# Optimization experiments

Measured on AMD Instinct MI355X. Metric: run time of the kernel, lower is better.

## Reference

```python
import jax, jax.numpy as jnp
import numpy as np

KH = KW = 3
STRIDE = 1
PAD = 1
DIL = 1
G = 4  # deformable groups


def setup_inputs() -> dict:
    key = jax.random.key(0)
    k1, k2, k3 = jax.random.split(key, 3)
    B, C, H, W = 8, 256, 64, 64
    K = KH * KW
    inp = jax.random.normal(k1, (B, C, H, W), dtype=jnp.float32)
    offset = jax.random.normal(k2, (B, 2 * G * K, H, W), dtype=jnp.float32)
    mask = jax.random.uniform(k3, (B, G * K, H, W), dtype=jnp.float32)
    return {"input": inp, "offset": offset, "mask": mask}


def _deform_sample(x, offset, mask):
    # x: [B,C,H,W]; offset: [B,2*G*K,Ho,Wo]; mask: [B,G*K,Ho,Wo]
    B, C, H, W = x.shape
    K = KH * KW
    Ho = (H + 2 * PAD - DIL * (KH - 1) - 1) // STRIDE + 1
    Wo = (W + 2 * PAD - DIL * (KW - 1) - 1) // STRIDE + 1
    Cg = C // G

    off = offset.reshape(B, G, K, 2, Ho, Wo)  # (dy, dx) per group/tap
    m = mask.reshape(B, G, K, Ho, Wo)

    # base sampling grid per kernel tap
    ky = (jnp.arange(KH) * DIL).repeat(KW)          # [K]
    kx = jnp.tile(jnp.arange(KW) * DIL, KH)          # [K]
    base_y = jnp.arange(Ho) * STRIDE - PAD           # [Ho]
    base_x = jnp.arange(Wo) * STRIDE - PAD           # [Wo]

    # sampling positions [B,G,K,Ho,Wo]
    py = base_y[None, None, None, :, None] + ky[None, None, :, None, None] + off[:, :, :, 0]
    px = base_x[None, None, None, None, :] + kx[None, None, :, None, None] + off[:, :, :, 1]

    y0 = jnp.floor(py).astype(jnp.int32)
    x0 = jnp.floor(px).astype(jnp.int32)
    ly = py - y0.astype(py.dtype)
    lx = px - x0.astype(px.dtype)

    xg = x.reshape(B, G, Cg, H * W)

    def gather(yy, xx, w):
        valid = (yy >= 0) & (yy < H) & (xx >= 0) & (xx < W)
        idx = jnp.clip(yy, 0, H - 1) * W + jnp.clip(xx, 0, W - 1)  # [B,G,K,Ho,Wo]
        g = jnp.take_along_axis(xg, idx.reshape(B, G, 1, -1), axis=3)
        g = g.reshape(B, G, Cg, K, Ho, Wo)
        return g * (w * valid.astype(w.dtype))[:, :, None]

    acc = gather(y0, x0, (1 - ly) * (1 - lx))
    acc = acc + gather(y0, x0 + 1, (1 - ly) * lx)
    acc = acc + gather(y0 + 1, x0, ly * (1 - lx))
    acc = acc + gather(y0 + 1, x0 + 1, ly * lx)

    # mask-weighted accumulation over kernel taps
    out = (acc * m[:, :, None]).sum(axis=3)  # [B,G,Cg,Ho,Wo]
    return out.reshape(B, C, Ho, Wo)


def reference(input, offset, mask):
    return _deform_sample(input, offset, mask)
```

## Files before the change

### kernel.cpp

```cpp
#include <hip/hip_runtime.h>
#include <hip/hip_fp16.h>

#define B_  8
#define C_  256
#define H_  64
#define W_  64
#define G_  4
#define CG_ 64
#define K_  9
#define HW_ (H_ * W_)

__global__ __launch_bounds__(256) void to_nhwc_f16(const float* __restrict__ in,
                                                   __half* __restrict__ out) {
  __shared__ unsigned int tile[32][65];
  const int b  = blockIdx.z;
  const int p0 = blockIdx.x * 64;
  const int c0 = blockIdx.y * 64;
  const int tid = threadIdx.x;
  const float* src = in + (size_t)b * C_ * HW_;
  __half* dst = out + (size_t)b * HW_ * C_;

  const int px = tid & 63;
  const int cp0 = tid >> 6;
#pragma unroll
  for (int i = 0; i < 8; ++i) {
    const int cp = cp0 + i * 4;
    const int c = c0 + cp * 2;
    const float v0 = src[(size_t)c * HW_ + p0 + px];
    const float v1 = src[(size_t)(c + 1) * HW_ + p0 + px];
    const unsigned int lo = (unsigned int)__half_as_ushort(__float2half(v0));
    const unsigned int hi = (unsigned int)__half_as_ushort(__float2half(v1));
    tile[cp][px] = lo | (hi << 16);
  }
  __syncthreads();

  const int cpair = tid & 31;
  const int pr0   = tid >> 5;
#pragma unroll
  for (int i = 0; i < 8; ++i) {
    const int p = pr0 + i * 8;
    *(unsigned int*)(dst + (size_t)(p0 + p) * C_ + c0 + 2 * cpair) = tile[cpair][p];
  }
}

__global__ __launch_bounds__(256) void deform_f16(const __half* __restrict__ x,
                                                  const float* __restrict__ off,
                                                  const float* __restrict__ msk,
                                                  float* __restrict__ out) {
  __shared__ int4   s_o[288];
  __shared__ float4 s_w[288];
  __shared__ float  s_out[CG_ * 33];

  const int wo0 = blockIdx.x * 32;
  const int ho  = blockIdx.y;
  const int b   = blockIdx.z >> 2;
  const int g   = blockIdx.z & 3;
  const int tid = threadIdx.x;

  for (int e = tid; e < 288; e += 256) {
    const int wi = e / 9, k = e - wi * 9;
    const int wo = wo0 + wi;
    const int ky = k / 3, kx = k - ky * 3;
    const int och = (g * K_ + k) * 2;
    const size_t ob = ((size_t)(b * (2 * G_ * K_) + och) * H_ + ho) * W_ + wo;
    const float dy = off[ob];
    const float dx = off[ob + HW_];
    const float m  = msk[((size_t)(b * (G_ * K_) + g * K_ + k) * H_ + ho) * W_ + wo];

    const float py = (float)(ho - 1 + ky) + dy;
    const float px = (float)(wo - 1 + kx) + dx;
    const float fy = floorf(py), fx = floorf(px);
    const int y0 = (int)fy, x0 = (int)fx;
    const int y1 = y0 + 1,  x1 = x0 + 1;
    const float ly = py - fy, lx = px - fx;

    const bool vy0 = ((unsigned)y0 < (unsigned)H_), vy1 = ((unsigned)y1 < (unsigned)H_);
    const bool vx0 = ((unsigned)x0 < (unsigned)W_), vx1 = ((unsigned)x1 < (unsigned)W_);
    const float wy0 = (1.f - ly) * m, wy1 = ly * m;

    float4 w;
    w.x = (vy0 && vx0) ? wy0 * (1.f - lx) : 0.f;
    w.y = (vy0 && vx1) ? wy0 * lx         : 0.f;
    w.z = (vy1 && vx0) ? wy1 * (1.f - lx) : 0.f;
    w.w = (vy1 && vx1) ? wy1 * lx         : 0.f;

    const int y0c = min(max(y0, 0), H_ - 1), y1c = min(max(y1, 0), H_ - 1);
    const int x0c = min(max(x0, 0), W_ - 1), x1c = min(max(x1, 0), W_ - 1);

    const int gb = g * CG_;
    int4 o;
    o.x = (y0c * W_ + x0c) * C_ + gb;
    o.y = (y0c * W_ + x1c) * C_ + gb;
    o.z = (y1c * W_ + x0c) * C_ + gb;
    o.w = (y1c * W_ + x1c) * C_ + gb;
    s_o[e] = o;
    s_w[e] = w;
  }
  __syncthreads();

  const int ci = tid & 7;
  const int wi = tid >> 3;
  const __half* xb = x + (size_t)b * (HW_ * C_) + ci * 8;

  float acc[8] = {0.f, 0.f, 0.f, 0.f, 0.f, 0.f, 0.f, 0.f};

#pragma unroll
  for (int k = 0; k < 9; ++k) {
    const int e = wi * 9 + k;
    const int4   o = s_o[e];
    const float4 w = s_w[e];
    const float4 r00 = *(const float4*)(xb + o.x);
    const float4 r01 = *(const float4*)(xb + o.y);
    const float4 r10 = *(const float4*)(xb + o.z);
    const float4 r11 = *(const float4*)(xb + o.w);
    const __half* h00 = (const __half*)&r00;
    const __half* h01 = (const __half*)&r01;
    const __half* h10 = (const __half*)&r10;
    const __half* h11 = (const __half*)&r11;
#pragma unroll
    for (int j = 0; j < 8; ++j) {
      float a = acc[j];
      a = fmaf(w.x, __half2float(h00[j]), a);
      a = fmaf(w.y, __half2float(h01[j]), a);
      a = fmaf(w.z, __half2float(h10[j]), a);
      a = fmaf(w.w, __half2float(h11[j]), a);
      acc[j] = a;
    }
  }

#pragma unroll
  for (int j = 0; j < 8; ++j) s_out[(ci * 8 + j) * 33 + wi] = acc[j];
  __syncthreads();

  float* ob = out + ((size_t)(b * C_ + g * CG_)) * HW_ + ho * W_ + wo0;
  const int wlane = tid & 31;
  const int cr    = tid >> 5;
#pragma unroll
  for (int q = 0; q < 8; ++q) {
    const int c = cr + q * 8;
    ob[(size_t)c * HW_ + wlane] = s_out[c * 33 + wlane];
  }
}

__global__ __launch_bounds__(256) void deform_f32_nchw(const float* __restrict__ x,
                                                       const float* __restrict__ off,
                                                       const float* __restrict__ msk,
                                                       float* __restrict__ out) {
  __shared__ int4   s_o[144];
  __shared__ float4 s_w[144];
  const int woq = blockIdx.x;
  const int ho  = blockIdx.y;
  const int b   = blockIdx.z >> 2;
  const int g   = blockIdx.z & 3;
  const int tid = threadIdx.x;

  if (tid < 144) {
    const int wi = tid / 9, k = tid - wi * 9;
    const int wo = woq * 16 + wi;
    const int ky = k / 3, kx = k - ky * 3;
    const int och = (g * K_ + k) * 2;
    const size_t ob = ((size_t)(b * (2 * G_ * K_) + och) * H_ + ho) * W_ + wo;
    const float dy = off[ob];
    const float dx = off[ob + HW_];
    const float m  = msk[((size_t)(b * (G_ * K_) + g * K_ + k) * H_ + ho) * W_ + wo];
    const float py = (float)(ho - 1 + ky) + dy;
    const float px = (float)(wo - 1 + kx) + dx;
    const float fy = floorf(py), fx = floorf(px);
    const int y0 = (int)fy, x0 = (int)fx;
    const int y1 = y0 + 1,  x1 = x0 + 1;
    const float ly = py - fy, lx = px - fx;
    const bool vy0 = ((unsigned)y0 < (unsigned)H_), vy1 = ((unsigned)y1 < (unsigned)H_);
    const bool vx0 = ((unsigned)x0 < (unsigned)W_), vx1 = ((unsigned)x1 < (unsigned)W_);
    const float wy0 = (1.f - ly) * m, wy1 = ly * m;
    float4 w;
    w.x = (vy0 && vx0) ? wy0 * (1.f - lx) : 0.f;
    w.y = (vy0 && vx1) ? wy0 * lx         : 0.f;
    w.z = (vy1 && vx0) ? wy1 * (1.f - lx) : 0.f;
    w.w = (vy1 && vx1) ? wy1 * lx         : 0.f;
    const int y0c = min(max(y0, 0), H_ - 1), y1c = min(max(y1, 0), H_ - 1);
    const int x0c = min(max(x0, 0), W_ - 1), x1c = min(max(x1, 0), W_ - 1);
    s_o[tid] = make_int4(y0c * W_ + x0c, y0c * W_ + x1c, y1c * W_ + x0c, y1c * W_ + x1c);
    s_w[tid] = w;
  }
  __syncthreads();

  const int ci = tid & 15, wi = tid >> 4;
  const float* xb = x + (size_t)(b * C_ + g * CG_ + ci * 4) * HW_;
  float a0 = 0.f, a1 = 0.f, a2 = 0.f, a3 = 0.f;
#pragma unroll
  for (int k = 0; k < 9; ++k) {
    const int e = wi * 9 + k;
    const int4   o = s_o[e];
    const float4 w = s_w[e];
    a0 += w.x * xb[o.x] + w.y * xb[o.y] + w.z * xb[o.z] + w.w * xb[o.w];
    const float* x1p = xb + HW_;
    a1 += w.x * x1p[o.x] + w.y * x1p[o.y] + w.z * x1p[o.z] + w.w * x1p[o.w];
    const float* x2p = xb + 2 * HW_;
    a2 += w.x * x2p[o.x] + w.y * x2p[o.y] + w.z * x2p[o.z] + w.w * x2p[o.w];
    const float* x3p = xb + 3 * HW_;
    a3 += w.x * x3p[o.x] + w.y * x3p[o.y] + w.z * x3p[o.z] + w.w * x3p[o.w];
  }
  float* ob = out + ((size_t)(b * C_ + g * CG_ + ci * 4)) * HW_ + ho * W_ + woq * 16 + wi;
  ob[0] = a0; ob[HW_] = a1; ob[2 * HW_] = a2; ob[3 * HW_] = a3;
}

extern "C" void kernel_launch(void* const* d_in, const int* in_sizes, int n_in,
                              void* d_out, int out_size, void* d_ws, size_t ws_size,
                              hipStream_t stream) {
  const float* inp = (const float*)d_in[0];
  const float* off = (const float*)d_in[1];
  const float* msk = (const float*)d_in[2];
  float* out = (float*)d_out;

  const size_t need = (size_t)B_ * C_ * HW_ * sizeof(__half);
  if (ws_size >= need) {
    __half* xt = (__half*)d_ws;
    to_nhwc_f16<<<dim3(HW_ / 64, C_ / 64, B_), 256, 0, stream>>>(inp, xt);
    deform_f16<<<dim3(2, H_, B_ * G_), 256, 0, stream>>>(xt, off, msk, out);
  } else {
    deform_f32_nchw<<<dim3(4, H_, B_ * G_), 256, 0, stream>>>(inp, off, msk, out);
  }
}
```

Baseline: 42.58 us.

## Use per-group GHWC fp16 layout and process full output rows per block

The transposed fp16 input is now laid out per deformable group (B,G,H,W,Cg), so each group's 64 channels for a pixel sit in one contiguous 128-byte run. Each block now covers a full 64-wide output row, and each thread accumulates two output columns to get more independent gathers in flight. The offset/mask prologue reads contiguous 64-pixel rows per tap, and shared memory for the staging and output transpose is overlapped through a union. The cost is fewer blocks (half the grid) and more registers per thread, which may lower occupancy.

```diff
diff --git a/kernel.cpp b/kernel.cpp
--- a/kernel.cpp
+++ b/kernel.cpp
@@ -10,22 +10,22 @@
 #define K_  9
 #define HW_ (H_ * W_)
 
-__global__ __launch_bounds__(256) void to_nhwc_f16(const float* __restrict__ in,
+__global__ __launch_bounds__(256) void to_ghwc_f16(const float* __restrict__ in,
                                                    __half* __restrict__ out) {
   __shared__ unsigned int tile[32][65];
   const int b  = blockIdx.z;
   const int p0 = blockIdx.x * 64;
-  const int c0 = blockIdx.y * 64;
+  const int g  = blockIdx.y;
   const int tid = threadIdx.x;
-  const float* src = in + (size_t)b * C_ * HW_;
-  __half* dst = out + (size_t)b * HW_ * C_;
-
-  const int px = tid & 63;
+  const float* src = in + (size_t)b * C_ * HW_ + (size_t)g * CG_ * HW_;
+  __half* dst = out + ((size_t)(b * G_ + g) * HW_) * CG_;
+
+  const int px  = tid & 63;
   const int cp0 = tid >> 6;
 #pragma unroll
   for (int i = 0; i < 8; ++i) {
     const int cp = cp0 + i * 4;
-    const int c = c0 + cp * 2;
+    const int c  = cp * 2;
     const float v0 = src[(size_t)c * HW_ + p0 + px];
     const float v1 = src[(size_t)(c + 1) * HW_ + p0 + px];
     const unsigned int lo = (unsigned int)__half_as_ushort(__float2half(v0));
@@ -39,40 +39,42 @@
 #pragma unroll
   for (int i = 0; i < 8; ++i) {
     const int p = pr0 + i * 8;
-    *(unsigned int*)(dst + (size_t)(p0 + p) * C_ + c0 + 2 * cpair) = tile[cpair][p];
-  }
-}
-
-__global__ __launch_bounds__(256) void deform_f16(const __half* __restrict__ x,
+    *(unsigned int*)(dst + (size_t)(p0 + p) * CG_ + 2 * cpair) = tile[cpair][p];
+  }
+}
+
+union DeformSM {
+  struct { int4 o[576]; float4 w[576]; } p;
+  float ot[64][65];
+};
+
+__global__ __launch_bounds__(256) void deform_g16(const __half* __restrict__ x,
                                                   const float* __restrict__ off,
                                                   const float* __restrict__ msk,
                                                   float* __restrict__ out) {
-  __shared__ int4   s_o[288];
-  __shared__ float4 s_w[288];
-  __shared__ float  s_out[CG_ * 33];
-
-  const int wo0 = blockIdx.x * 32;
-  const int ho  = blockIdx.y;
-  const int b   = blockIdx.z >> 2;
-  const int g   = blockIdx.z & 3;
+  __shared__ DeformSM sm;
+
+  const int ho  = blockIdx.x;
+  const int b   = blockIdx.y >> 2;
+  const int g   = blockIdx.y & 3;
   const int tid = threadIdx.x;
 
-  for (int e = tid; e < 288; e += 256) {
-    const int wi = e / 9, k = e - wi * 9;
-    const int wo = wo0 + wi;
+  for (int e = tid; e < 576; e += 256) {
+    const int px = e & 63;
+    const int k  = e >> 6;
     const int ky = k / 3, kx = k - ky * 3;
     const int och = (g * K_ + k) * 2;
-    const size_t ob = ((size_t)(b * (2 * G_ * K_) + och) * H_ + ho) * W_ + wo;
+    const size_t ob = ((size_t)(b * (2 * G_ * K_) + och) * HW_) + ho * W_ + px;
     const float dy = off[ob];
     const float dx = off[ob + HW_];
-    const float m  = msk[((size_t)(b * (G_ * K_) + g * K_ + k) * H_ + ho) * W_ + wo];
+    const float m  = msk[((size_t)(b * (G_ * K_) + g * K_ + k) * HW_) + ho * W_ + px];
 
     const float py = (float)(ho - 1 + ky) + dy;
-    const float px = (float)(wo - 1 + kx) + dx;
-    const float fy = floorf(py), fx = floorf(px);
+    const float pxx = (float)(px - 1 + kx) + dx;
+    const float fy = floorf(py), fx = floorf(pxx);
     const int y0 = (int)fy, x0 = (int)fx;
     const int y1 = y0 + 1,  x1 = x0 + 1;
-    const float ly = py - fy, lx = px - fx;
+    const float ly = py - fy, lx = pxx - fx;
 
     const bool vy0 = ((unsigned)y0 < (unsigned)H_), vy1 = ((unsigned)y1 < (unsigned)H_);
     const bool vx0 = ((unsigned)x0 < (unsigned)W_), vx1 = ((unsigned)x1 < (unsigned)W_);
@@ -87,58 +89,79 @@
     const int y0c = min(max(y0, 0), H_ - 1), y1c = min(max(y1, 0), H_ - 1);
     const int x0c = min(max(x0, 0), W_ - 1), x1c = min(max(x1, 0), W_ - 1);
 
-    const int gb = g * CG_;
     int4 o;
-    o.x = (y0c * W_ + x0c) * C_ + gb;
-    o.y = (y0c * W_ + x1c) * C_ + gb;
-    o.z = (y1c * W_ + x0c) * C_ + gb;
-    o.w = (y1c * W_ + x1c) * C_ + gb;
-    s_o[e] = o;
-    s_w[e] = w;
+    o.x = (y0c * W_ + x0c) << 7;
+    o.y = (y0c * W_ + x1c) << 7;
+    o.z = (y1c * W_ + x0c) << 7;
+    o.w = (y1c * W_ + x1c) << 7;
+    sm.p.o[e] = o;
+    sm.p.w[e] = w;
   }
   __syncthreads();
 
   const int ci = tid & 7;
   const int wi = tid >> 3;
-  const __half* xb = x + (size_t)b * (HW_ * C_) + ci * 8;
-
-  float acc[8] = {0.f, 0.f, 0.f, 0.f, 0.f, 0.f, 0.f, 0.f};
+  const char* xb = (const char*)x + (size_t)(b * G_ + g) * HW_ * CG_ * 2 + ci * 16;
+
+  float a0[8] = {0.f, 0.f, 0.f, 0.f, 0.f, 0.f, 0.f, 0.f};
+  float a1[8] = {0.f, 0.f, 0.f, 0.f, 0.f, 0.f, 0.f, 0.f};
 
 #pragma unroll
   for (int k = 0; k < 9; ++k) {
-    const int e = wi * 9 + k;
-    const int4   o = s_o[e];
-    const float4 w = s_w[e];
-    const float4 r00 = *(const float4*)(xb + o.x);
-    const float4 r01 = *(const float4*)(xb + o.y);
-    const float4 r10 = *(const float4*)(xb + o.z);
-    const float4 r11 = *(const float4*)(xb + o.w);
-    const __half* h00 = (const __half*)&r00;
-    const __half* h01 = (const __half*)&r01;
-    const __half* h10 = (const __half*)&r10;
-    const __half* h11 = (const __half*)&r11;
+    const int4   oA = sm.p.o[k * 64 + wi];
+    const float4 wA = sm.p.w[k * 64 + wi];
+    const int4   oB = sm.p.o[k * 64 + wi + 32];
+    const float4 wB = sm.p.w[k * 64 + wi + 32];
+
+    const float4 rA0 = *(const float4*)(xb + oA.x);
+    const float4 rA1 = *(const float4*)(xb + oA.y);
+    const float4 rA2 = *(const float4*)(xb + oA.z);
+    const float4 rA3 = *(const float4*)(xb + oA.w);
+    const float4 rB0 = *(const float4*)(xb + oB.x);
+    const float4 rB1 = *(const float4*)(xb + oB.y);
+    const float4 rB2 = *(const float4*)(xb + oB.z);
+    const float4 rB3 = *(const float4*)(xb + oB.w);
+
+    const __half* hA0 = (const __half*)&rA0;
+    const __half* hA1 = (const __half*)&rA1;
+    const __half* hA2 = (const __half*)&rA2;
+    const __half* hA3 = (const __half*)&rA3;
+    const __half* hB0 = (const __half*)&rB0;
+    const __half* hB1 = (const __half*)&rB1;
+    const __half* hB2 = (const __half*)&rB2;
+    const __half* hB3 = (const __half*)&rB3;
 #pragma unroll
     for (int j = 0; j < 8; ++j) {
-      float a = acc[j];
-      a = fmaf(w.x, __half2float(h00[j]), a);
-      a = fmaf(w.y, __half2float(h01[j]), a);
-      a = fmaf(w.z, __half2float(h10[j]), a);
-      a = fmaf(w.w, __half2float(h11[j]), a);
-      acc[j] = a;
+      float s0 = a0[j];
+      s0 = fmaf(wA.x, __half2float(hA0[j]), s0);
+      s0 = fmaf(wA.y, __half2float(hA1[j]), s0);
+      s0 = fmaf(wA.z, __half2float(hA2[j]), s0);
+      s0 = fmaf(wA.w, __half2float(hA3[j]), s0);
+      a0[j] = s0;
+      float s1 = a1[j];
+      s1 = fmaf(wB.x, __half2float(hB0[j]), s1);
+      s1 = fmaf(wB.y, __half2float(hB1[j]), s1);
+      s1 = fmaf(wB.z, __half2float(hB2[j]), s1);
+      s1 = fmaf(wB.w, __half2float(hB3[j]), s1);
+      a1[j] = s1;
     }
   }
 
-#pragma unroll
-  for (int j = 0; j < 8; ++j) s_out[(ci * 8 + j) * 33 + wi] = acc[j];
-  __syncthreads();
-
-  float* ob = out + ((size_t)(b * C_ + g * CG_)) * HW_ + ho * W_ + wo0;
-  const int wlane = tid & 31;
-  const int cr    = tid >> 5;
-#pragma unroll
-  for (int q = 0; q < 8; ++q) {
-    const int c = cr + q * 8;
-    ob[(size_t)c * HW_ + wlane] = s_out[c * 33 + wlane];
+  __syncthreads();
+#pragma unroll
+  for (int j = 0; j < 8; ++j) {
+    sm.ot[ci * 8 + j][wi]      = a0[j];
+    sm.ot[ci * 8 + j][wi + 32] = a1[j];
+  }
+  __syncthreads();
+
+  float* ob = out + ((size_t)(b * C_ + g * CG_)) * HW_ + ho * W_;
+  const int lane = tid & 63;
+  const int r0   = tid >> 6;
+#pragma unroll
+  for (int q = 0; q < 16; ++q) {
+    const int c = q * 4 + r0;
+    ob[(size_t)c * HW_ + lane] = sm.ot[c][lane];
   }
 }
 
@@ -215,8 +238,8 @@
   const size_t need = (size_t)B_ * C_ * HW_ * sizeof(__half);
   if (ws_size >= need) {
     __half* xt = (__half*)d_ws;
-    to_nhwc_f16<<<dim3(HW_ / 64, C_ / 64, B_), 256, 0, stream>>>(inp, xt);
-    deform_f16<<<dim3(2, H_, B_ * G_), 256, 0, stream>>>(xt, off, msk, out);
+    to_ghwc_f16<<<dim3(HW_ / 64, G_, B_), 256, 0, stream>>>(inp, xt);
+    deform_g16<<<dim3(H_, B_ * G_), 256, 0, stream>>>(xt, off, msk, out);
   } else {
     deform_f32_nchw<<<dim3(4, H_, B_ * G_), 256, 0, stream>>>(inp, off, msk, out);
   }
```

After: 45.93 us. 1.08x slower.
